# Kernel tuning notes

Hardware: AMD Instinct MI355X
Metric: run time of the kernel (lower is better)

Reference implementation:

```python
import jax, jax.numpy as jnp
import numpy as np

B, D, QL, DL, E, V, NB = 32, 8, 16, 512, 300, 50000, 5
EPS = 1e-8  # torch cosine_similarity eps
# numpy.histogram edges [-1.0,-0.5,0,0.5,1.0,1.0] -> 5 bins, last bin [1.0,1.0] inclusive
BIN_LO = jnp.array([-1.0, -0.5, 0.0, 0.5, 1.0], dtype=jnp.float32)
BIN_HI = jnp.array([-0.5, 0.0, 0.5, 1.0, 1.0], dtype=jnp.float32)


def setup_inputs() -> dict:
    key = jax.random.key(0)
    ks = jax.random.split(key, 12)
    batch_queries = jax.random.randint(ks[0], (B, QL), 0, V)
    query_len = jax.random.randint(ks[1], (B,), 1, QL)
    batch_docs = jax.random.randint(ks[2], (B, D, DL), 0, V)
    doc_len = jax.random.randint(ks[3], (B, D), 1, DL)
    emb = jax.random.normal(ks[4], (V, E), dtype=jnp.float32) * 0.1
    emb = emb.at[0].set(0.0)  # PAD row (padding_idx)
    w_g = jax.random.normal(ks[5], (E, 1), dtype=jnp.float32) * 0.05
    b_g = jnp.zeros((1,), dtype=jnp.float32)
    w1 = jax.random.normal(ks[6], (NB, 1), dtype=jnp.float32) * 0.3
    b1 = jnp.zeros((1,), dtype=jnp.float32)
    w2 = jax.random.normal(ks[7], (1, 1), dtype=jnp.float32)
    b2 = jnp.zeros((1,), dtype=jnp.float32)
    w_o = jax.random.normal(ks[8], (1, 1), dtype=jnp.float32)
    b_o = jnp.zeros((1,), dtype=jnp.float32)
    return {"batch_queries": batch_queries, "query_len": query_len,
            "batch_docs": batch_docs, "doc_len": doc_len,
            "emb": emb, "w_g": w_g, "b_g": b_g, "w1": w1, "b1": b1,
            "w2": w2, "b2": b2, "w_o": w_o, "b_o": b_o}


def _histogram(cos):
    # cos: [N, qlen, dlen] -> counts [N, qlen, 5] (numpy.histogram semantics)
    v = cos[..., None]                              # [N,q,d,1]
    hi_ok = jnp.concatenate([v[..., :1] < BIN_HI[:4], v[..., :1] <= BIN_HI[4:]], axis=-1)
    mask = (v >= BIN_LO) & hi_ok                    # [N,q,d,5]
    return mask.astype(jnp.float32).sum(axis=2)     # [N,q,5]


def reference(batch_queries, query_len, batch_docs, doc_len,
              emb, w_g, b_g, w1, b1, w2, b2, w_o, b_o):
    q_emb = emb[batch_queries]                      # [B,q,E]
    # gating network: Linear(E,1) -> softmax over query terms
    gate = (q_emb @ w_g).squeeze(-1) + b_g          # [B,q]
    term_weights = jax.nn.softmax(gate, axis=1)     # [B,q]
    term_weights = jnp.broadcast_to(term_weights[:, None, :], (B, D, QL))

    d_emb = emb[batch_docs.reshape(B * D, DL)]      # [N,d,E]
    q_rep = jnp.broadcast_to(q_emb[:, None], (B, D, QL, E)).reshape(B * D, QL, E)

    # cosine similarity without materializing the replicated [N,q,d,E] tensors
    dots = jnp.einsum('nqe,nde->nqd', q_rep, d_emb)
    qn = jnp.linalg.norm(q_rep, axis=-1)            # [N,q]
    dn = jnp.linalg.norm(d_emb, axis=-1)            # [N,d]
    cos = dots / jnp.maximum(qn[:, :, None] * dn[:, None, :], EPS)

    # histogram feats are detached in the original (cpu numpy round-trip)
    hist = jax.lax.stop_gradient(_histogram(cos))   # [N,q,5]

    ffnn = ((hist @ w1 + b1) @ w2 + b2).squeeze(-1) # [N,q]
    ffnn = ffnn.reshape(B, D, QL)
    weighted = ffnn * term_weights                  # [B,D,q]
    s = weighted.sum(axis=2, keepdims=True)         # [B,D,1]
    score = (s @ w_o + b_o).squeeze(-1)             # [B,D]
    return score
```

## Files before the change

### kernel.cpp

```cpp
#include <hip/hip_runtime.h>


constexpr int Bn  = 32;
constexpr int Dn  = 8;
constexpr int QLn = 16;
constexpr int DLn = 512;
constexpr int En  = 300;

__global__ __launch_bounds__(256) void drmm_score(
    const int*   __restrict__ bq,
    const int*   __restrict__ bd,
    const float* __restrict__ emb,
    const float* __restrict__ w_g,
    const float* __restrict__ b_g,
    const float* __restrict__ w1,
    const float* __restrict__ b1,
    const float* __restrict__ w2,
    const float* __restrict__ b2,
    const float* __restrict__ w_o,
    const float* __restrict__ b_o,
    float*       __restrict__ out)
{
    __shared__ __attribute__((aligned(16))) float q_lds[QLn * En];
    __shared__ float pn_s[QLn][17];
    __shared__ float pg_s[QLn][17];
    __shared__ float qn_s[QLn];
    __shared__ float gate_s[QLn];
    __shared__ float tw_s[QLn];
    __shared__ unsigned long long hist_s[QLn];
    __shared__ float wsum_s[QLn];

    const int n   = blockIdx.x;
    const int b   = n >> 3;
    const int tid = threadIdx.x;

    for (int idx = tid; idx < QLn * (En / 4); idx += 256) {
        const int  q   = idx / (En / 4);
        const int  c   = idx - q * (En / 4);
        const long tok = bq[b * QLn + q];
        *reinterpret_cast<float4*>(&q_lds[q * En + c * 4]) =
            *reinterpret_cast<const float4*>(emb + tok * (long)En + c * 4);
    }
    if (tid < QLn) hist_s[tid] = 0ull;
    __syncthreads();

    {
        const int q = tid >> 4, j = tid & 15;
        float pn = 0.f, pg = 0.f;
        for (int e = j; e < En; e += 16) {
            const float v = q_lds[q * En + e];
            pn = fmaf(v, v, pn);
            pg = fmaf(v, w_g[e], pg);
        }
        pn_s[q][j] = pn;
        pg_s[q][j] = pg;
    }
    __syncthreads();
    if (tid < QLn) {
        float sn = 0.f, sg = 0.f;
        for (int j = 0; j < 16; ++j) { sn += pn_s[tid][j]; sg += pg_s[tid][j]; }
        qn_s[tid]   = sqrtf(sn);
        gate_s[tid] = sg + b_g[0];
    }
    __syncthreads();
    if (tid == 0) {
        float m = gate_s[0];
        for (int q = 1; q < QLn; ++q) m = fmaxf(m, gate_s[q]);
        float ex[QLn];
        float s = 0.f;
        for (int q = 0; q < QLn; ++q) { ex[q] = expf(gate_s[q] - m); s += ex[q]; }
        for (int q = 0; q < QLn; ++q) tw_s[q] = ex[q] / s;
    }
    __syncthreads();

    const long tok0 = bd[n * DLn + tid];
    const long tok1 = bd[n * DLn + tid + 256];
    const float* __restrict__ r0 = emb + tok0 * (long)En;
    const float* __restrict__ r1 = emb + tok1 * (long)En;

    float acc0[QLn], acc1[QLn];
#pragma unroll
    for (int q = 0; q < QLn; ++q) { acc0[q] = 0.f; acc1[q] = 0.f; }
    float nr0 = 0.f, nr1 = 0.f;

#define DRMM_CHUNK(d0, d1, EE)                                            \
    do {                                                                  \
        nr0 = fmaf((d0).x, (d0).x, nr0);                                  \
        nr0 = fmaf((d0).y, (d0).y, nr0);                                  \
        nr0 = fmaf((d0).z, (d0).z, nr0);                                  \
        nr0 = fmaf((d0).w, (d0).w, nr0);                                  \
        nr1 = fmaf((d1).x, (d1).x, nr1);                                  \
        nr1 = fmaf((d1).y, (d1).y, nr1);                                  \
        nr1 = fmaf((d1).z, (d1).z, nr1);                                  \
        nr1 = fmaf((d1).w, (d1).w, nr1);                                  \
        _Pragma("unroll")                                                 \
        for (int q = 0; q < QLn; ++q) {                                   \
            const float4 qv =                                             \
                *reinterpret_cast<const float4*>(&q_lds[q * En + (EE)]);  \
            float s0 = acc0[q];                                           \
            s0 = fmaf((d0).x, qv.x, s0);                                  \
            s0 = fmaf((d0).y, qv.y, s0);                                  \
            s0 = fmaf((d0).z, qv.z, s0);                                  \
            s0 = fmaf((d0).w, qv.w, s0);                                  \
            acc0[q] = s0;                                                 \
            float s1 = acc1[q];                                           \
            s1 = fmaf((d1).x, qv.x, s1);                                  \
            s1 = fmaf((d1).y, qv.y, s1);                                  \
            s1 = fmaf((d1).z, qv.z, s1);                                  \
            s1 = fmaf((d1).w, qv.w, s1);                                  \
            acc1[q] = s1;                                                 \
        }                                                                 \
    } while (0)

#define DRMM_STEP_R(SA, SB, EE)                                           \
    do {                                                                  \
        DRMM_CHUNK(SA, SB, (EE));                                         \
        SA = *reinterpret_cast<const float4*>(r0 + (EE) + 20);            \
        SB = *reinterpret_cast<const float4*>(r1 + (EE) + 20);            \
    } while (0)

    float4 s0a = *reinterpret_cast<const float4*>(r0 + 0);
    float4 s1a = *reinterpret_cast<const float4*>(r1 + 0);
    float4 s0b = *reinterpret_cast<const float4*>(r0 + 4);
    float4 s1b = *reinterpret_cast<const float4*>(r1 + 4);
    float4 s0c = *reinterpret_cast<const float4*>(r0 + 8);
    float4 s1c = *reinterpret_cast<const float4*>(r1 + 8);
    float4 s0d = *reinterpret_cast<const float4*>(r0 + 12);
    float4 s1d = *reinterpret_cast<const float4*>(r1 + 12);
    float4 s0e = *reinterpret_cast<const float4*>(r0 + 16);
    float4 s1e = *reinterpret_cast<const float4*>(r1 + 16);

#pragma unroll 1
    for (int k = 0; k < 14; ++k) {
        const int e = k * 20;
        DRMM_STEP_R(s0a, s1a, e + 0);
        DRMM_STEP_R(s0b, s1b, e + 4);
        DRMM_STEP_R(s0c, s1c, e + 8);
        DRMM_STEP_R(s0d, s1d, e + 12);
        DRMM_STEP_R(s0e, s1e, e + 16);
    }
    DRMM_CHUNK(s0a, s1a, 280);
    DRMM_CHUNK(s0b, s1b, 284);
    DRMM_CHUNK(s0c, s1c, 288);
    DRMM_CHUNK(s0d, s1d, 292);
    DRMM_CHUNK(s0e, s1e, 296);
#undef DRMM_STEP_R
#undef DRMM_CHUNK

    const float dn0 = sqrtf(nr0);
    const float dn1 = sqrtf(nr1);

    unsigned long long cnt[QLn];
#pragma unroll
    for (int q = 0; q < QLn; ++q) {
        unsigned long long v = 0ull;
        {
            const float denom = fmaxf(qn_s[q] * dn0, 1e-8f);
            const float c     = acc0[q] / denom;
            int bin = -1;
            if      (c >= -1.0f && c < -0.5f) bin = 0;
            else if (c >= -0.5f && c <  0.0f) bin = 1;
            else if (c >=  0.0f && c <  0.5f) bin = 2;
            else if (c >=  0.5f && c <  1.0f) bin = 3;
            else if (c ==  1.0f)              bin = 4;
            if (bin >= 0) v += 1ull << (12 * bin);
        }
        {
            const float denom = fmaxf(qn_s[q] * dn1, 1e-8f);
            const float c     = acc1[q] / denom;
            int bin = -1;
            if      (c >= -1.0f && c < -0.5f) bin = 0;
            else if (c >= -0.5f && c <  0.0f) bin = 1;
            else if (c >=  0.0f && c <  0.5f) bin = 2;
            else if (c >=  0.5f && c <  1.0f) bin = 3;
            else if (c ==  1.0f)              bin = 4;
            if (bin >= 0) v += 1ull << (12 * bin);
        }
        cnt[q] = v;
    }

    const int lane = tid & 63;
#pragma unroll
    for (int q = 0; q < QLn; ++q) {
        unsigned long long v = cnt[q];
        for (int off = 32; off > 0; off >>= 1) v += __shfl_down(v, off, 64);
        if (lane == 0) atomicAdd(&hist_s[q], v);
    }
    __syncthreads();

    if (tid < QLn) {
        const unsigned long long h = hist_s[tid];
        float f = 0.f;
        f = fmaf((float)((h >>  0) & 0xFFFull), w1[0], f);
        f = fmaf((float)((h >> 12) & 0xFFFull), w1[1], f);
        f = fmaf((float)((h >> 24) & 0xFFFull), w1[2], f);
        f = fmaf((float)((h >> 36) & 0xFFFull), w1[3], f);
        f = fmaf((float)((h >> 48) & 0xFFFull), w1[4], f);
        f += b1[0];
        f = f * w2[0] + b2[0];
        wsum_s[tid] = f * tw_s[tid];
    }
    __syncthreads();
    if (tid == 0) {
        float s = 0.f;
        for (int q = 0; q < QLn; ++q) s += wsum_s[q];
        out[n] = s * w_o[0] + b_o[0];
    }
}

extern "C" void kernel_launch(void* const* d_in, const int* in_sizes, int n_in,
                              void* d_out, int out_size, void* d_ws, size_t ws_size,
                              hipStream_t stream) {
    const int*   bq  = (const int*)  d_in[0];
    const int*   bd  = (const int*)  d_in[2];
    const float* emb = (const float*)d_in[4];
    const float* w_g = (const float*)d_in[5];
    const float* b_g = (const float*)d_in[6];
    const float* w1  = (const float*)d_in[7];
    const float* b1  = (const float*)d_in[8];
    const float* w2  = (const float*)d_in[9];
    const float* b2  = (const float*)d_in[10];
    const float* w_o = (const float*)d_in[11];
    const float* b_o = (const float*)d_in[12];

    drmm_score<<<Bn * Dn, 256, 0, stream>>>(
        bq, bd, emb, w_g, b_g, w1, b1, w2, b2, w_o, b_o, (float*)d_out);
}
```

Before: 60.17 us.

## Stage document embeddings through double-buffered LDS with register prefetch

Replaces the per-thread register rolling prefetch of document rows with a double-buffered LDS staging scheme. Each phase loads 20 floats per row into registers, computes on the previous LDS buffer, then writes the next buffer and synchronizes. The goal is to overlap global loads with the dot-product FMAs. In exchange it adds about 80 KB of LDS, extra LDS traffic and a block barrier per phase, with no data reuse across threads.

```diff
diff --git a/kernel.cpp b/kernel.cpp
--- a/kernel.cpp
+++ b/kernel.cpp
@@ -6,6 +6,8 @@
 constexpr int QLn = 16;
 constexpr int DLn = 512;
 constexpr int En  = 300;
+constexpr int PH  = 20;
+constexpr int NPH = 15;
 
 __global__ __launch_bounds__(256) void drmm_score(
     const int*   __restrict__ bq,
@@ -22,6 +24,7 @@
     float*       __restrict__ out)
 {
     __shared__ __attribute__((aligned(16))) float q_lds[QLn * En];
+    __shared__ float4 dlds4[2][5 * DLn];
     __shared__ float pn_s[QLn][17];
     __shared__ float pg_s[QLn][17];
     __shared__ float qn_s[QLn];
@@ -112,39 +115,70 @@
         }                                                                 \
     } while (0)
 
-#define DRMM_STEP_R(SA, SB, EE)                                           \
-    do {                                                                  \
-        DRMM_CHUNK(SA, SB, (EE));                                         \
-        SA = *reinterpret_cast<const float4*>(r0 + (EE) + 20);            \
-        SB = *reinterpret_cast<const float4*>(r1 + (EE) + 20);            \
-    } while (0)
-
-    float4 s0a = *reinterpret_cast<const float4*>(r0 + 0);
-    float4 s1a = *reinterpret_cast<const float4*>(r1 + 0);
-    float4 s0b = *reinterpret_cast<const float4*>(r0 + 4);
-    float4 s1b = *reinterpret_cast<const float4*>(r1 + 4);
-    float4 s0c = *reinterpret_cast<const float4*>(r0 + 8);
-    float4 s1c = *reinterpret_cast<const float4*>(r1 + 8);
-    float4 s0d = *reinterpret_cast<const float4*>(r0 + 12);
-    float4 s1d = *reinterpret_cast<const float4*>(r1 + 12);
-    float4 s0e = *reinterpret_cast<const float4*>(r0 + 16);
-    float4 s1e = *reinterpret_cast<const float4*>(r1 + 16);
+    float4 l00, l01, l02, l03, l04, l10, l11, l12, l13, l14;
+
+#define STAGE_LOAD(PP)                                                    \
+    do {                                                                  \
+        const int eb_ = (PP) * PH;                                        \
+        l00 = *reinterpret_cast<const float4*>(r0 + eb_ +  0);            \
+        l01 = *reinterpret_cast<const float4*>(r0 + eb_ +  4);            \
+        l02 = *reinterpret_cast<const float4*>(r0 + eb_ +  8);            \
+        l03 = *reinterpret_cast<const float4*>(r0 + eb_ + 12);            \
+        l04 = *reinterpret_cast<const float4*>(r0 + eb_ + 16);            \
+        l10 = *reinterpret_cast<const float4*>(r1 + eb_ +  0);            \
+        l11 = *reinterpret_cast<const float4*>(r1 + eb_ +  4);            \
+        l12 = *reinterpret_cast<const float4*>(r1 + eb_ +  8);            \
+        l13 = *reinterpret_cast<const float4*>(r1 + eb_ + 12);            \
+        l14 = *reinterpret_cast<const float4*>(r1 + eb_ + 16);            \
+    } while (0)
+
+#define STAGE_WRITE(PP)                                                   \
+    do {                                                                  \
+        float4* dst_ = &dlds4[(PP) & 1][0];                               \
+        dst_[0 * DLn + tid]       = l00;                                  \
+        dst_[1 * DLn + tid]       = l01;                                  \
+        dst_[2 * DLn + tid]       = l02;                                  \
+        dst_[3 * DLn + tid]       = l03;                                  \
+        dst_[4 * DLn + tid]       = l04;                                  \
+        dst_[0 * DLn + tid + 256] = l10;                                  \
+        dst_[1 * DLn + tid + 256] = l11;                                  \
+        dst_[2 * DLn + tid + 256] = l12;                                  \
+        dst_[3 * DLn + tid + 256] = l13;                                  \
+        dst_[4 * DLn + tid + 256] = l14;                                  \
+    } while (0)
+
+#define PHASE_COMPUTE(PP)                                                 \
+    do {                                                                  \
+        const float4* src_ = &dlds4[(PP) & 1][0];                         \
+        const int e0_ = (PP) * PH;                                        \
+        { float4 d0 = src_[0 * DLn + tid], d1 = src_[0 * DLn + tid + 256];\
+          DRMM_CHUNK(d0, d1, e0_ +  0); }                                 \
+        { float4 d0 = src_[1 * DLn + tid], d1 = src_[1 * DLn + tid + 256];\
+          DRMM_CHUNK(d0, d1, e0_ +  4); }                                 \
+        { float4 d0 = src_[2 * DLn + tid], d1 = src_[2 * DLn + tid + 256];\
+          DRMM_CHUNK(d0, d1, e0_ +  8); }                                 \
+        { float4 d0 = src_[3 * DLn + tid], d1 = src_[3 * DLn + tid + 256];\
+          DRMM_CHUNK(d0, d1, e0_ + 12); }                                 \
+        { float4 d0 = src_[4 * DLn + tid], d1 = src_[4 * DLn + tid + 256];\
+          DRMM_CHUNK(d0, d1, e0_ + 16); }                                 \
+    } while (0)
+
+    STAGE_LOAD(0);
+    STAGE_WRITE(0);
+    __syncthreads();
 
 #pragma unroll 1
-    for (int k = 0; k < 14; ++k) {
-        const int e = k * 20;
-        DRMM_STEP_R(s0a, s1a, e + 0);
-        DRMM_STEP_R(s0b, s1b, e + 4);
-        DRMM_STEP_R(s0c, s1c, e + 8);
-        DRMM_STEP_R(s0d, s1d, e + 12);
-        DRMM_STEP_R(s0e, s1e, e + 16);
-    }
-    DRMM_CHUNK(s0a, s1a, 280);
-    DRMM_CHUNK(s0b, s1b, 284);
-    DRMM_CHUNK(s0c, s1c, 288);
-    DRMM_CHUNK(s0d, s1d, 292);
-    DRMM_CHUNK(s0e, s1e, 296);
-#undef DRMM_STEP_R
+    for (int p = 0; p < NPH - 1; ++p) {
+        STAGE_LOAD(p + 1);
+        PHASE_COMPUTE(p);
+        STAGE_WRITE(p + 1);
+        __syncthreads();
+    }
+    PHASE_COMPUTE(NPH - 1);
+
+#undef PHASE_COMPUTE
+#undef STAGE_WRITE
+#undef STAGE_LOAD
 #undef DRMM_CHUNK
 
     const float dn0 = sqrtf(nr0);
```

New measurement: 75.76 us. +25.9%, slower.

## Split query terms across two blocks per doc and add a finalize kernel

Applied to the files above, without the earlier changes.

The main kernel now launches two blocks per (batch,doc) pair, each handling half of the query terms. Per-term histograms go to a workspace, and a second kernel computes the gating softmax and the final score. The goal is to double the grid from 256 blocks to 512 so the many CUs on the device are filled, and to cut accumulator register pressure from 32 to 16 per thread. In exchange, each doc embedding row is gathered twice, a second launch is added, and the histograms make a global-memory round trip.

```diff
diff --git a/kernel.cpp b/kernel.cpp
--- a/kernel.cpp
+++ b/kernel.cpp
@@ -4,72 +4,52 @@
 constexpr int Bn  = 32;
 constexpr int Dn  = 8;
 constexpr int QLn = 16;
+constexpr int QH  = 8;
 constexpr int DLn = 512;
 constexpr int En  = 300;
 
-__global__ __launch_bounds__(256) void drmm_score(
+__global__ __launch_bounds__(256) void drmm_partial(
     const int*   __restrict__ bq,
     const int*   __restrict__ bd,
     const float* __restrict__ emb,
-    const float* __restrict__ w_g,
-    const float* __restrict__ b_g,
-    const float* __restrict__ w1,
-    const float* __restrict__ b1,
-    const float* __restrict__ w2,
-    const float* __restrict__ b2,
-    const float* __restrict__ w_o,
-    const float* __restrict__ b_o,
-    float*       __restrict__ out)
+    unsigned long long* __restrict__ ws_hist)
 {
-    __shared__ __attribute__((aligned(16))) float q_lds[QLn * En];
-    __shared__ float pn_s[QLn][17];
-    __shared__ float pg_s[QLn][17];
-    __shared__ float qn_s[QLn];
-    __shared__ float gate_s[QLn];
-    __shared__ float tw_s[QLn];
-    __shared__ unsigned long long hist_s[QLn];
-    __shared__ float wsum_s[QLn];
-
-    const int n   = blockIdx.x;
-    const int b   = n >> 3;
-    const int tid = threadIdx.x;
-
-    for (int idx = tid; idx < QLn * (En / 4); idx += 256) {
+    __shared__ __attribute__((aligned(16))) float q_lds[QH * En];
+    __shared__ float pn_s[QH][17];
+    __shared__ float qn_s[QH];
+    __shared__ unsigned long long hist_s[QH];
+
+    const int bid  = blockIdx.x;
+    const int n    = bid & 255;
+    const int h    = bid >> 8;
+    const int qoff = h * QH;
+    const int b    = n >> 3;
+    const int tid  = threadIdx.x;
+
+    for (int idx = tid; idx < QH * (En / 4); idx += 256) {
         const int  q   = idx / (En / 4);
         const int  c   = idx - q * (En / 4);
-        const long tok = bq[b * QLn + q];
+        const long tok = bq[b * QLn + qoff + q];
         *reinterpret_cast<float4*>(&q_lds[q * En + c * 4]) =
             *reinterpret_cast<const float4*>(emb + tok * (long)En + c * 4);
     }
-    if (tid < QLn) hist_s[tid] = 0ull;
-    __syncthreads();
-
-    {
+    if (tid < QH) hist_s[tid] = 0ull;
+    __syncthreads();
+
+    if (tid < QH * 16) {
         const int q = tid >> 4, j = tid & 15;
-        float pn = 0.f, pg = 0.f;
+        float pn = 0.f;
         for (int e = j; e < En; e += 16) {
             const float v = q_lds[q * En + e];
             pn = fmaf(v, v, pn);
-            pg = fmaf(v, w_g[e], pg);
         }
         pn_s[q][j] = pn;
-        pg_s[q][j] = pg;
-    }
-    __syncthreads();
-    if (tid < QLn) {
-        float sn = 0.f, sg = 0.f;
-        for (int j = 0; j < 16; ++j) { sn += pn_s[tid][j]; sg += pg_s[tid][j]; }
-        qn_s[tid]   = sqrtf(sn);
-        gate_s[tid] = sg + b_g[0];
-    }
-    __syncthreads();
-    if (tid == 0) {
-        float m = gate_s[0];
-        for (int q = 1; q < QLn; ++q) m = fmaxf(m, gate_s[q]);
-        float ex[QLn];
-        float s = 0.f;
-        for (int q = 0; q < QLn; ++q) { ex[q] = expf(gate_s[q] - m); s += ex[q]; }
-        for (int q = 0; q < QLn; ++q) tw_s[q] = ex[q] / s;
+    }
+    __syncthreads();
+    if (tid < QH) {
+        float sn = 0.f;
+        for (int j = 0; j < 16; ++j) sn += pn_s[tid][j];
+        qn_s[tid] = sqrtf(sn);
     }
     __syncthreads();
 
@@ -78,9 +58,9 @@
     const float* __restrict__ r0 = emb + tok0 * (long)En;
     const float* __restrict__ r1 = emb + tok1 * (long)En;
 
-    float acc0[QLn], acc1[QLn];
+    float acc0[QH], acc1[QH];
 #pragma unroll
-    for (int q = 0; q < QLn; ++q) { acc0[q] = 0.f; acc1[q] = 0.f; }
+    for (int q = 0; q < QH; ++q) { acc0[q] = 0.f; acc1[q] = 0.f; }
     float nr0 = 0.f, nr1 = 0.f;
 
 #define DRMM_CHUNK(d0, d1, EE)                                            \
@@ -94,7 +74,7 @@
         nr1 = fmaf((d1).z, (d1).z, nr1);                                  \
         nr1 = fmaf((d1).w, (d1).w, nr1);                                  \
         _Pragma("unroll")                                                 \
-        for (int q = 0; q < QLn; ++q) {                                   \
+        for (int q = 0; q < QH; ++q) {                                    \
             const float4 qv =                                             \
                 *reinterpret_cast<const float4*>(&q_lds[q * En + (EE)]);  \
             float s0 = acc0[q];                                           \
@@ -150,9 +130,9 @@
     const float dn0 = sqrtf(nr0);
     const float dn1 = sqrtf(nr1);
 
-    unsigned long long cnt[QLn];
+    unsigned long long cnt[QH];
 #pragma unroll
-    for (int q = 0; q < QLn; ++q) {
+    for (int q = 0; q < QH; ++q) {
         unsigned long long v = 0ull;
         {
             const float denom = fmaxf(qn_s[q] * dn0, 1e-8f);
@@ -181,21 +161,71 @@
 
     const int lane = tid & 63;
 #pragma unroll
-    for (int q = 0; q < QLn; ++q) {
+    for (int q = 0; q < QH; ++q) {
         unsigned long long v = cnt[q];
         for (int off = 32; off > 0; off >>= 1) v += __shfl_down(v, off, 64);
         if (lane == 0) atomicAdd(&hist_s[q], v);
     }
     __syncthreads();
 
+    if (tid < QH) ws_hist[n * QLn + qoff + tid] = hist_s[tid];
+}
+
+__global__ __launch_bounds__(256) void drmm_final(
+    const int*   __restrict__ bq,
+    const float* __restrict__ emb,
+    const float* __restrict__ w_g,
+    const float* __restrict__ b_g,
+    const unsigned long long* __restrict__ ws_hist,
+    const float* __restrict__ w1,
+    const float* __restrict__ b1,
+    const float* __restrict__ w2,
+    const float* __restrict__ b2,
+    const float* __restrict__ w_o,
+    const float* __restrict__ b_o,
+    float*       __restrict__ out)
+{
+    __shared__ float pg_s[QLn][17];
+    __shared__ float gate_s[QLn];
+    __shared__ float tw_s[QLn];
+    __shared__ float wsum_s[QLn];
+
+    const int n   = blockIdx.x;
+    const int b   = n >> 3;
+    const int tid = threadIdx.x;
+
+    {
+        const int  q   = tid >> 4, j = tid & 15;
+        const long tok = bq[b * QLn + q];
+        const float* __restrict__ row = emb + tok * (long)En;
+        float pg = 0.f;
+        for (int e = j; e < En; e += 16) pg = fmaf(row[e], w_g[e], pg);
+        pg_s[q][j] = pg;
+    }
+    __syncthreads();
     if (tid < QLn) {
-        const unsigned long long h = hist_s[tid];
+        float sg = 0.f;
+        for (int j = 0; j < 16; ++j) sg += pg_s[tid][j];
+        gate_s[tid] = sg + b_g[0];
+    }
+    __syncthreads();
+    if (tid == 0) {
+        float m = gate_s[0];
+        for (int q = 1; q < QLn; ++q) m = fmaxf(m, gate_s[q]);
+        float ex[QLn];
+        float s = 0.f;
+        for (int q = 0; q < QLn; ++q) { ex[q] = expf(gate_s[q] - m); s += ex[q]; }
+        for (int q = 0; q < QLn; ++q) tw_s[q] = ex[q] / s;
+    }
+    __syncthreads();
+    if (tid < QLn) {
+        const unsigned long long hh = ws_hist[n * QLn + tid];
         float f = 0.f;
-        f = fmaf((float)((h >>  0) & 0xFFFull), w1[0], f);
-        f = fmaf((float)((h >> 12) & 0xFFFull), w1[1], f);
-        f = fmaf((float)((h >> 24) & 0xFFFull), w1[2], f);
-        f = fmaf((float)((h >> 36) & 0xFFFull), w1[3], f);
-        f = fmaf((float)((h >> 48) & 0xFFFull), w1[4], f);
+        f = fmaf((float)((hh >>  0) & 0xFFFull), w1[0], f);
+        f = fmaf((float)((hh >> 12) & 0xFFFull), w1[1], f);
+        f = fmaf((float)((hh >> 24) & 0xFFFull), w1[2], f);
+        f = fmaf((float)((hh >> 36) & 0xFFFull), w1[3], f);
+        f = fmaf((float)((hh >> 48) & 0xFFFull), w1[4], f);
         f += b1[0];
         f = f * w2[0] + b2[0];
         wsum_s[tid] = f * tw_s[tid];
@@ -223,6 +253,9 @@
     const float* w_o = (const float*)d_in[11];
     const float* b_o = (const float*)d_in[12];
 
-    drmm_score<<<Bn * Dn, 256, 0, stream>>>(
-        bq, bd, emb, w_g, b_g, w1, b1, w2, b2, w_o, b_o, (float*)d_out);
+    unsigned long long* ws_hist = (unsigned long long*)d_ws;
+
+    drmm_partial<<<Bn * Dn * 2, 256, 0, stream>>>(bq, bd, emb, ws_hist);
+    drmm_final<<<Bn * Dn, 256, 0, stream>>>(
+        bq, emb, w_g, b_g, ws_hist, w1, b1, w2, b2, w_o, b_o, (float*)d_out);
 }
```

Result: slower. 88.38 us (+46.9%).
